# Performance work log

Hardware: AMD Instinct MI355X
Metric: run time of the kernel (lower is better)

Reference implementation:

```python
import jax, jax.numpy as jnp
import numpy as np

B, N, H = 8, 2048, 256

def setup_inputs() -> dict:
    key = jax.random.key(0)
    k1, k2, k3, k4, k5 = jax.random.split(key, 5)
    h = jax.random.normal(k1, (B, N, H), dtype=jnp.float32)
    node_mask = jnp.ones((B, N, 1), dtype=jnp.float32)
    n_nodes = N  # unused by the forward math, kept for signature fidelity
    s1 = 1.0 / np.sqrt(H)
    W1 = jax.random.uniform(k2, (H, H), minval=-s1, maxval=s1, dtype=jnp.float32)
    b1 = jax.random.uniform(k3, (H,), minval=-s1, maxval=s1, dtype=jnp.float32)
    w2 = jax.random.uniform(k4, (H,), minval=-s1, maxval=s1, dtype=jnp.float32)
    b2 = jax.random.uniform(k5, (), minval=-s1, maxval=s1, dtype=jnp.float32)
    return {"h": h, "node_mask": node_mask, "n_nodes": n_nodes,
            "W1": W1, "b1": b1, "w2": w2, "b2": b2}

def reference(h, node_mask, n_nodes, W1, b1, w2, b2):
    # node_dec: Linear + SiLU
    x = jax.nn.silu(jnp.einsum('bnh,oh->bno', h, W1) + b1)  # [B,N,H]
    # pre_di applied to pairwise difference is linear, so factor:
    # pre_di(x_i - x_j) = (x_i @ w2) - (x_j @ w2) + b2
    s = jnp.einsum('bnh,h->bn', x, w2)                       # [B,N]
    out = s[:, :, None] - s[:, None, :] + b2                 # [B,N,N]
    return out.astype(jnp.int64)                             # torch .long() truncates
```

## Files before the change

### kernel.cpp

```cpp
#include <hip/hip_runtime.h>
#include <math.h>

#define B_ 8
#define N_ 2048
#define H_ 256

typedef double d4 __attribute__((ext_vector_type(4)));

__global__ __launch_bounds__(256)
void transpose_w1(const float* __restrict__ W1, float* __restrict__ W1T) {
    W1T[(size_t)blockIdx.x * H_ + threadIdx.x] =
        W1[(size_t)threadIdx.x * H_ + blockIdx.x];
}

__device__ __forceinline__ int self_probe_var() {
    const int l = threadIdx.x & 63;
    d4 z = {0.0, 0.0, 0.0, 0.0};
    d4 r1 = __builtin_amdgcn_mfma_f64_16x16x4f64((double)(l + 1), 1.0, z, 0, 0, 0);
    d4 r2 = __builtin_amdgcn_mfma_f64_16x16x4f64(1.0, (double)(l + 1), z, 0, 0, 0);
    d4 r3 = __builtin_amdgcn_mfma_f64_16x16x4f64((double)(l & 15), 1.0, z, 0, 0, 0);
    const double pw0 = __shfl(r1[0], 0, 64);
    const double pw1 = __shfl(r2[0], 0, 64);
    const double pw2 = __shfl(r3[0], 1, 64);
    const double pw3 = __shfl(r3[2], 16, 64);
    const double pw4 = __shfl(r2[2], 16, 64);
    if (pw0 != 100.0 || pw1 != 100.0) return 0;
    if (pw2 == 0.0 && pw3 == 24.0)  return 1;
    if (pw2 == 0.0 && pw3 == 36.0)  return 3;
    if (pw2 == 4.0 && pw4 == 124.0) return 2;
    if (pw2 == 4.0 && pw4 == 136.0) return 4;
    return 0;
}

__global__ __launch_bounds__(256)
__attribute__((amdgpu_waves_per_eu(2, 4)))
void s_mfma_uni(const float* __restrict__ hp, const float* __restrict__ W1T,
                const float* __restrict__ b1, const float* __restrict__ w2,
                double* __restrict__ s_out) {
    const int var = self_probe_var();
    if (var == 0) return;
    __shared__ double spart[4][32];
    const int t = threadIdx.x;
    const int lane = t & 63;
    const int wave = __builtin_amdgcn_readfirstlane(t >> 6);
    const int a15 = lane & 15, g = lane >> 4;
    const int m0 = blockIdx.x * 32;
    const int oc = wave * 64;
    const float* ap0 = hp + (size_t)(m0 + a15) * H_ + g;
    const float* ap1 = hp + (size_t)(m0 + 16 + a15) * H_ + g;
    const float* bp  = W1T + (size_t)g * H_ + oc + a15;

    d4 acc[2][4];
    #pragma unroll
    for (int mt = 0; mt < 2; ++mt)
        #pragma unroll
        for (int ot = 0; ot < 4; ++ot) acc[mt][ot] = (d4){0.0, 0.0, 0.0, 0.0};

    float ac[4], an[4];
    float bcv[8], bnv[8];
    ac[0] = ap0[0]; ac[1] = ap0[4]; ac[2] = ap1[0]; ac[3] = ap1[4];
    #pragma unroll
    for (int ot = 0; ot < 4; ++ot) {
        bcv[ot]     = bp[ot * 16];
        bcv[4 + ot] = bp[4 * H_ + ot * 16];
    }

    for (int kc = 0; kc < H_; kc += 8) {
        const int kn = (kc + 8 < H_) ? (kc + 8) : 0;
        an[0] = ap0[kn]; an[1] = ap0[kn + 4];
        an[2] = ap1[kn]; an[3] = ap1[kn + 4];
        #pragma unroll
        for (int ot = 0; ot < 4; ++ot) {
            bnv[ot]     = bp[(size_t)kn * H_ + ot * 16];
            bnv[4 + ot] = bp[(size_t)(kn + 4) * H_ + ot * 16];
        }
        {
            const double a0 = (double)ac[0], a1 = (double)ac[2];
            #pragma unroll
            for (int ot = 0; ot < 4; ++ot) {
                const double bv = (double)bcv[ot];
                acc[0][ot] = __builtin_amdgcn_mfma_f64_16x16x4f64(a0, bv, acc[0][ot], 0, 0, 0);
                acc[1][ot] = __builtin_amdgcn_mfma_f64_16x16x4f64(a1, bv, acc[1][ot], 0, 0, 0);
            }
        }
        {
            const double a0 = (double)ac[1], a1 = (double)ac[3];
            #pragma unroll
            for (int ot = 0; ot < 4; ++ot) {
                const double bv = (double)bcv[4 + ot];
                acc[0][ot] = __builtin_amdgcn_mfma_f64_16x16x4f64(a0, bv, acc[0][ot], 0, 0, 0);
                acc[1][ot] = __builtin_amdgcn_mfma_f64_16x16x4f64(a1, bv, acc[1][ot], 0, 0, 0);
            }
        }
        #pragma unroll
        for (int q = 0; q < 4; ++q) ac[q] = an[q];
        #pragma unroll
        for (int q = 0; q < 8; ++q) bcv[q] = bnv[q];
    }

    if (var == 1 || var == 3) {
        double psum[2][4];
        #pragma unroll
        for (int mt = 0; mt < 2; ++mt)
            #pragma unroll
            for (int v = 0; v < 4; ++v) psum[mt][v] = 0.0;
        #pragma unroll
        for (int ot = 0; ot < 4; ++ot) {
            const int o = oc + ot * 16 + a15;
            const double bb = (double)b1[o];
            const double ww = (double)w2[o];
            #pragma unroll
            for (int mt = 0; mt < 2; ++mt)
                #pragma unroll
                for (int v = 0; v < 4; ++v) {
                    const double u = acc[mt][ot][v] + bb;
                    psum[mt][v] += ww * (u / (1.0 + exp(-u)));
                }
        }
        #pragma unroll
        for (int mt = 0; mt < 2; ++mt)
            #pragma unroll
            for (int v = 0; v < 4; ++v) {
                double x = psum[mt][v];
                x += __shfl_xor(x, 1, 64);
                x += __shfl_xor(x, 2, 64);
                x += __shfl_xor(x, 4, 64);
                x += __shfl_xor(x, 8, 64);
                psum[mt][v] = x;
            }
        if (a15 == 0) {
            #pragma unroll
            for (int mt = 0; mt < 2; ++mt)
                #pragma unroll
                for (int v = 0; v < 4; ++v) {
                    const int row = (var == 1) ? (4 * g + v) : (g + 4 * v);
                    spart[wave][mt * 16 + row] = psum[mt][v];
                }
        }
    } else {
        double ps[2] = {0.0, 0.0};
        #pragma unroll
        for (int ot = 0; ot < 4; ++ot)
            #pragma unroll
            for (int v = 0; v < 4; ++v) {
                const int cv = (var == 2) ? (4 * g + v) : (g + 4 * v);
                const int o = oc + ot * 16 + cv;
                const double bb = (double)b1[o];
                const double ww = (double)w2[o];
                #pragma unroll
                for (int mt = 0; mt < 2; ++mt) {
                    const double u = acc[mt][ot][v] + bb;
                    ps[mt] += ww * (u / (1.0 + exp(-u)));
                }
            }
        #pragma unroll
        for (int mt = 0; mt < 2; ++mt) {
            ps[mt] += __shfl_xor(ps[mt], 16, 64);
            ps[mt] += __shfl_xor(ps[mt], 32, 64);
        }
        if (g == 0) {
            spart[wave][a15]      = ps[0];
            spart[wave][16 + a15] = ps[1];
        }
    }
    __syncthreads();
    if (t < 32)
        s_out[m0 + t] = spart[0][t] + spart[1][t] + spart[2][t] + spart[3][t];
}

__global__ __launch_bounds__(256)
__attribute__((amdgpu_waves_per_eu(2, 4)))
void s_valu_kernel(const float* __restrict__ hp, const float* __restrict__ W1T,
                   const float* __restrict__ b1, const float* __restrict__ w2,
                   double* __restrict__ s_out) {
    if (self_probe_var() != 0) return;
    const int t = threadIdx.x;
    const int lane = t & 63;
    const int wave = __builtin_amdgcn_readfirstlane(t >> 6);
    const int m0 = blockIdx.x * 16 + wave * 4;
    const int o0 = lane * 4;
    const float* hr = hp + (size_t)m0 * H_;
    const float* wp = W1T + o0;

    double acc[4][4];
    #pragma unroll
    for (int j = 0; j < 4; ++j)
        #pragma unroll
        for (int r = 0; r < 4; ++r) acc[j][r] = 0.0;

    float4 wA[8], wB[8];
    float hA[32], hB[32];

    #define LOADW(dst, kcv)                                                   \
        do {                                                                  \
            _Pragma("unroll")                                                 \
            for (int kk = 0; kk < 8; ++kk)                                    \
                dst[kk] = *reinterpret_cast<const float4*>(                   \
                    wp + (size_t)((kcv) + kk) * H_);                          \
        } while (0)

    #define LOADH(dst, kcv)                                                   \
        do {                                                                  \
            _Pragma("unroll")                                                 \
            for (int r = 0; r < 4; ++r)                                       \
                _Pragma("unroll")                                             \
                for (int kk = 0; kk < 8; ++kk)                                \
                    dst[r * 8 + kk] = hr[r * H_ + (kcv) + kk];                \
        } while (0)

    #define COMPUTE(wv, hbuf)                                                 \
        do {                                                                  \
            _Pragma("unroll")                                                 \
            for (int kk = 0; kk < 8; ++kk) {                                  \
                const double h0 = (double)hbuf[0 * 8 + kk];                   \
                const double h1 = (double)hbuf[1 * 8 + kk];                   \
                const double h2 = (double)hbuf[2 * 8 + kk];                   \
                const double h3 = (double)hbuf[3 * 8 + kk];                   \
                const double a0 = (double)wv[kk].x;                           \
                const double a1 = (double)wv[kk].y;                           \
                const double a2 = (double)wv[kk].z;                           \
                const double a3 = (double)wv[kk].w;                           \
                acc[0][0] = fma(a0, h0, acc[0][0]);                           \
                acc[0][1] = fma(a0, h1, acc[0][1]);                           \
                acc[0][2] = fma(a0, h2, acc[0][2]);                           \
                acc[0][3] = fma(a0, h3, acc[0][3]);                           \
                acc[1][0] = fma(a1, h0, acc[1][0]);                           \
                acc[1][1] = fma(a1, h1, acc[1][1]);                           \
                acc[1][2] = fma(a1, h2, acc[1][2]);                           \
                acc[1][3] = fma(a1, h3, acc[1][3]);                           \
                acc[2][0] = fma(a2, h0, acc[2][0]);                           \
                acc[2][1] = fma(a2, h1, acc[2][1]);                           \
                acc[2][2] = fma(a2, h2, acc[2][2]);                           \
                acc[2][3] = fma(a2, h3, acc[2][3]);                           \
                acc[3][0] = fma(a3, h0, acc[3][0]);                           \
                acc[3][1] = fma(a3, h1, acc[3][1]);                           \
                acc[3][2] = fma(a3, h2, acc[3][2]);                           \
                acc[3][3] = fma(a3, h3, acc[3][3]);                           \
            }                                                                 \
        } while (0)

    LOADW(wA, 0);
    LOADH(hA, 0);
    for (int kc = 0; kc < H_; kc += 16) {
        LOADW(wB, kc + 8);
        LOADH(hB, kc + 8);
        COMPUTE(wA, hA);
        if (kc + 16 < H_) {
            LOADW(wA, kc + 16);
            LOADH(hA, kc + 16);
        }
        COMPUTE(wB, hB);
    }
    #undef LOADW
    #undef LOADH
    #undef COMPUTE

    const float4 b1v = *reinterpret_cast<const float4*>(b1 + o0);
    const float4 w2v = *reinterpret_cast<const float4*>(w2 + o0);
    double psum[4] = {0.0, 0.0, 0.0, 0.0};
    #define EPI(j, bc, wc)                                                    \
        do {                                                                  \
            const double bb = (double)bc, ww = (double)wc;                    \
            _Pragma("unroll")                                                 \
            for (int r = 0; r < 4; ++r) {                                     \
                const double u = acc[j][r] + bb;                              \
                psum[r] += ww * (u / (1.0 + exp(-u)));                        \
            }                                                                 \
        } while (0)
    EPI(0, b1v.x, w2v.x);
    EPI(1, b1v.y, w2v.y);
    EPI(2, b1v.z, w2v.z);
    EPI(3, b1v.w, w2v.w);
    #undef EPI

    #pragma unroll
    for (int r = 0; r < 4; ++r) {
        double v = psum[r];
        v += __shfl_xor(v, 1, 64);
        v += __shfl_xor(v, 2, 64);
        v += __shfl_xor(v, 4, 64);
        v += __shfl_xor(v, 8, 64);
        v += __shfl_xor(v, 16, 64);
        v += __shfl_xor(v, 32, 64);
        if (lane == 0) s_out[m0 + r] = v;
    }
}

__global__ __launch_bounds__(256)
void pair_kernel(const double* __restrict__ s, const float* __restrict__ b2p,
                 int* __restrict__ out) {
    const double b2 = (double)b2p[0];
    const unsigned total4 = (unsigned)(B_) * (unsigned)(N_) * (unsigned)(N_) / 4u;
    const unsigned stride = gridDim.x * blockDim.x;
    for (unsigned idx = blockIdx.x * blockDim.x + threadIdx.x; idx < total4;
         idx += stride) {
        const unsigned base = idx * 4u;
        const unsigned bi  = base >> 22;
        const unsigned rem = base & ((1u << 22) - 1u);
        const unsigned i   = rem >> 11;
        const unsigned j   = rem & (N_ - 1u);
        const double si = s[bi * N_ + i];
        const double* sp = s + bi * N_ + j;
        const double sj0 = sp[0], sj1 = sp[1], sj2 = sp[2], sj3 = sp[3];
        int4 o;
        o.x = (int)trunc((si - sj0) + b2);
        o.y = (int)trunc((si - sj1) + b2);
        o.z = (int)trunc((si - sj2) + b2);
        o.w = (int)trunc((si - sj3) + b2);
        *reinterpret_cast<int4*>(out + base) = o;
    }
}

extern "C" void kernel_launch(void* const* d_in, const int* in_sizes, int n_in,
                              void* d_out, int out_size, void* d_ws, size_t ws_size,
                              hipStream_t stream) {
    const float* hp = (const float*)d_in[0];
    const float* W1 = (const float*)d_in[3];
    const float* b1 = (const float*)d_in[4];
    const float* w2 = (const float*)d_in[5];
    const float* b2 = (const float*)d_in[6];

    float*  W1T = (float*)d_ws;
    double* s   = (double*)((char*)d_ws + H_ * H_ * sizeof(float));
    int* out = (int*)d_out;

    transpose_w1<<<H_, H_, 0, stream>>>(W1, W1T);
    s_mfma_uni<<<(B_ * N_) / 32, 256, 0, stream>>>(hp, W1T, b1, w2, s);
    s_valu_kernel<<<(B_ * N_) / 16, 256, 0, stream>>>(hp, W1T, b1, w2, s);
    pair_kernel<<<2048, 256, 0, stream>>>(s, b2, out);
}
```

Baseline: 74.62 us.

## Pack W1 into a per-lane contiguous layout for float4 B-operand loads

Adds a pack_w1 kernel that reorders W1 rows so that each lane's K-slices for its output column sit contiguously. The MFMA GEMM loop can then fetch B operands with float4 loads over 16 chunks instead of strided scalar loads, and the K indexing is permuted so each lane covers k = g + 4*(...) groups. The intent is fewer, wider memory instructions in the inner loop. The cost is an extra launch and more workspace, and the per-lane A loads become strided by 4 floats.

```diff
diff --git a/kernel.cpp b/kernel.cpp
--- a/kernel.cpp
+++ b/kernel.cpp
@@ -11,6 +11,12 @@
 void transpose_w1(const float* __restrict__ W1, float* __restrict__ W1T) {
     W1T[(size_t)blockIdx.x * H_ + threadIdx.x] =
         W1[(size_t)threadIdx.x * H_ + blockIdx.x];
+}
+
+__global__ __launch_bounds__(256)
+void pack_w1(const float* __restrict__ W1, float* __restrict__ W1P) {
+    const int o = blockIdx.x, k = threadIdx.x;
+    W1P[(size_t)o * H_ + (k & 3) * 64 + (k >> 2)] = W1[(size_t)o * H_ + k];
 }
 
 __device__ __forceinline__ int self_probe_var() {
@@ -34,7 +40,7 @@
 
 __global__ __launch_bounds__(256)
 __attribute__((amdgpu_waves_per_eu(2, 4)))
-void s_mfma_uni(const float* __restrict__ hp, const float* __restrict__ W1T,
+void s_mfma_uni(const float* __restrict__ hp, const float* __restrict__ W1P,
                 const float* __restrict__ b1, const float* __restrict__ w2,
                 double* __restrict__ s_out) {
     const int var = self_probe_var();
@@ -47,8 +53,8 @@
     const int m0 = blockIdx.x * 32;
     const int oc = wave * 64;
     const float* ap0 = hp + (size_t)(m0 + a15) * H_ + g;
-    const float* ap1 = hp + (size_t)(m0 + 16 + a15) * H_ + g;
-    const float* bp  = W1T + (size_t)g * H_ + oc + a15;
+    const float* ap1 = ap0 + 16 * H_;
+    const float* bq = W1P + ((size_t)(oc + a15) * 4 + g) * 64;
 
     d4 acc[2][4];
     #pragma unroll
@@ -56,47 +62,64 @@
         #pragma unroll
         for (int ot = 0; ot < 4; ++ot) acc[mt][ot] = (d4){0.0, 0.0, 0.0, 0.0};
 
-    float ac[4], an[4];
-    float bcv[8], bnv[8];
-    ac[0] = ap0[0]; ac[1] = ap0[4]; ac[2] = ap1[0]; ac[3] = ap1[4];
-    #pragma unroll
-    for (int ot = 0; ot < 4; ++ot) {
-        bcv[ot]     = bp[ot * 16];
-        bcv[4 + ot] = bp[4 * H_ + ot * 16];
-    }
-
-    for (int kc = 0; kc < H_; kc += 8) {
-        const int kn = (kc + 8 < H_) ? (kc + 8) : 0;
-        an[0] = ap0[kn]; an[1] = ap0[kn + 4];
-        an[2] = ap1[kn]; an[3] = ap1[kn + 4];
-        #pragma unroll
-        for (int ot = 0; ot < 4; ++ot) {
-            bnv[ot]     = bp[(size_t)kn * H_ + ot * 16];
-            bnv[4 + ot] = bp[(size_t)(kn + 4) * H_ + ot * 16];
-        }
-        {
-            const double a0 = (double)ac[0], a1 = (double)ac[2];
-            #pragma unroll
-            for (int ot = 0; ot < 4; ++ot) {
-                const double bv = (double)bcv[ot];
-                acc[0][ot] = __builtin_amdgcn_mfma_f64_16x16x4f64(a0, bv, acc[0][ot], 0, 0, 0);
-                acc[1][ot] = __builtin_amdgcn_mfma_f64_16x16x4f64(a1, bv, acc[1][ot], 0, 0, 0);
-            }
-        }
-        {
-            const double a0 = (double)ac[1], a1 = (double)ac[3];
-            #pragma unroll
-            for (int ot = 0; ot < 4; ++ot) {
-                const double bv = (double)bcv[4 + ot];
-                acc[0][ot] = __builtin_amdgcn_mfma_f64_16x16x4f64(a0, bv, acc[0][ot], 0, 0, 0);
-                acc[1][ot] = __builtin_amdgcn_mfma_f64_16x16x4f64(a1, bv, acc[1][ot], 0, 0, 0);
-            }
-        }
-        #pragma unroll
-        for (int q = 0; q < 4; ++q) ac[q] = an[q];
-        #pragma unroll
-        for (int q = 0; q < 8; ++q) bcv[q] = bnv[q];
-    }
+    float4 bc[4], bn[4];
+    float ac[8], an[8];
+
+    #define LOADB(dst, c)                                                     \
+        do {                                                                  \
+            _Pragma("unroll")                                                 \
+            for (int ot = 0; ot < 4; ++ot)                                    \
+                dst[ot] = *reinterpret_cast<const float4*>(                   \
+                    bq + ot * 16 * H_ * 4 / 4 * 4 / 4 + 0);                   \
+        } while (0)
+    #undef LOADB
+    #define LOADB(dst, c)                                                     \
+        do {                                                                  \
+            _Pragma("unroll")                                                 \
+            for (int ot = 0; ot < 4; ++ot)                                    \
+                dst[ot] = *reinterpret_cast<const float4*>(                   \
+                    bq + (size_t)ot * 4096 + (c) * 4);                        \
+        } while (0)
+
+    #define LOADA(dst, c)                                                     \
+        do {                                                                  \
+            _Pragma("unroll")                                                 \
+            for (int q = 0; q < 4; ++q) {                                     \
+                dst[q]     = ap0[(c) * 16 + q * 4];                           \
+                dst[4 + q] = ap1[(c) * 16 + q * 4];                           \
+            }                                                                 \
+        } while (0)
+
+    LOADB(bc, 0);
+    LOADA(ac, 0);
+    for (int c = 0; c < 16; ++c) {
+        const int cn = (c + 1 < 16) ? (c + 1) : 0;
+        LOADB(bn, cn);
+        LOADA(an, cn);
+        #pragma unroll
+        for (int q = 0; q < 4; ++q) {
+            const double a0 = (double)ac[q];
+            const double a1 = (double)ac[4 + q];
+            const double b0 = (double)((const float*)&bc[0])[q];
+            const double b1v = (double)((const float*)&bc[1])[q];
+            const double b2v = (double)((const float*)&bc[2])[q];
+            const double b3v = (double)((const float*)&bc[3])[q];
+            acc[0][0] = __builtin_amdgcn_mfma_f64_16x16x4f64(a0, b0,  acc[0][0], 0, 0, 0);
+            acc[1][0] = __builtin_amdgcn_mfma_f64_16x16x4f64(a1, b0,  acc[1][0], 0, 0, 0);
+            acc[0][1] = __builtin_amdgcn_mfma_f64_16x16x4f64(a0, b1v, acc[0][1], 0, 0, 0);
+            acc[1][1] = __builtin_amdgcn_mfma_f64_16x16x4f64(a1, b1v, acc[1][1], 0, 0, 0);
+            acc[0][2] = __builtin_amdgcn_mfma_f64_16x16x4f64(a0, b2v, acc[0][2], 0, 0, 0);
+            acc[1][2] = __builtin_amdgcn_mfma_f64_16x16x4f64(a1, b2v, acc[1][2], 0, 0, 0);
+            acc[0][3] = __builtin_amdgcn_mfma_f64_16x16x4f64(a0, b3v, acc[0][3], 0, 0, 0);
+            acc[1][3] = __builtin_amdgcn_mfma_f64_16x16x4f64(a1, b3v, acc[1][3], 0, 0, 0);
+        }
+        #pragma unroll
+        for (int q = 0; q < 8; ++q) ac[q] = an[q];
+        #pragma unroll
+        for (int q = 0; q < 4; ++q) bc[q] = bn[q];
+    }
+    #undef LOADB
+    #undef LOADA
 
     if (var == 1 || var == 3) {
         double psum[2][4];
@@ -321,11 +344,13 @@
     const float* b2 = (const float*)d_in[6];
 
     float*  W1T = (float*)d_ws;
-    double* s   = (double*)((char*)d_ws + H_ * H_ * sizeof(float));
+    float*  W1P = (float*)((char*)d_ws + 256 * 1024);
+    double* s   = (double*)((char*)d_ws + 512 * 1024);
     int* out = (int*)d_out;
 
     transpose_w1<<<H_, H_, 0, stream>>>(W1, W1T);
-    s_mfma_uni<<<(B_ * N_) / 32, 256, 0, stream>>>(hp, W1T, b1, w2, s);
+    pack_w1<<<H_, H_, 0, stream>>>(W1, W1P);
+    s_mfma_uni<<<(B_ * N_) / 32, 256, 0, stream>>>(hp, W1P, b1, w2, s);
     s_valu_kernel<<<(B_ * N_) / 16, 256, 0, stream>>>(hp, W1T, b1, w2, s);
     pair_kernel<<<2048, 256, 0, stream>>>(s, b2, out);
 }
```

Measured after the change: 89.49 us. 19.9% more time.

## Split K across two wave groups in fp64 MFMA kernel with LDS reduction

Applied to the files above, without the earlier changes.

Doubles the block to 512 threads and splits the 256-wide K dimension between two groups of four waves. Each group accumulates half of the fp64 MFMA products, and the first group writes its partials to a 64KB LDS buffer that the second group adds before the SiLU and w2 epilogue. The goal is to halve the serial MFMA chain per wave and raise latency hiding. In exchange it adds an LDS round trip, an extra barrier and a large shared-memory footprint that may cap occupancy.

```diff
diff --git a/kernel.cpp b/kernel.cpp
--- a/kernel.cpp
+++ b/kernel.cpp
@@ -32,23 +32,27 @@
     return 0;
 }
 
-__global__ __launch_bounds__(256)
+__global__ __launch_bounds__(512)
 __attribute__((amdgpu_waves_per_eu(2, 4)))
 void s_mfma_uni(const float* __restrict__ hp, const float* __restrict__ W1T,
                 const float* __restrict__ b1, const float* __restrict__ w2,
                 double* __restrict__ s_out) {
     const int var = self_probe_var();
     if (var == 0) return;
+    __shared__ double u_lds[4][32][64];
     __shared__ double spart[4][32];
     const int t = threadIdx.x;
     const int lane = t & 63;
-    const int wave = __builtin_amdgcn_readfirstlane(t >> 6);
+    const int w = __builtin_amdgcn_readfirstlane(t >> 6);
+    const int kh = w >> 2;
+    const int ow = w & 3;
     const int a15 = lane & 15, g = lane >> 4;
     const int m0 = blockIdx.x * 32;
-    const int oc = wave * 64;
-    const float* ap0 = hp + (size_t)(m0 + a15) * H_ + g;
-    const float* ap1 = hp + (size_t)(m0 + 16 + a15) * H_ + g;
-    const float* bp  = W1T + (size_t)g * H_ + oc + a15;
+    const int oc = ow * 64;
+    const int K0 = kh * 128;
+    const float* ap0 = hp + (size_t)(m0 + a15) * H_ + g + K0;
+    const float* ap1 = ap0 + 16 * H_;
+    const float* bp  = W1T + (size_t)(K0 + g) * H_ + oc + a15;
 
     d4 acc[2][4];
     #pragma unroll
@@ -65,8 +69,8 @@
         bcv[4 + ot] = bp[4 * H_ + ot * 16];
     }
 
-    for (int kc = 0; kc < H_; kc += 8) {
-        const int kn = (kc + 8 < H_) ? (kc + 8) : 0;
+    for (int kc = 0; kc < 128; kc += 8) {
+        const int kn = (kc + 8 < 128) ? (kc + 8) : 0;
         an[0] = ap0[kn]; an[1] = ap0[kn + 4];
         an[2] = ap1[kn]; an[3] = ap1[kn + 4];
         #pragma unroll
@@ -98,69 +102,89 @@
         for (int q = 0; q < 8; ++q) bcv[q] = bnv[q];
     }
 
-    if (var == 1 || var == 3) {
-        double psum[2][4];
+    if (kh == 0) {
         #pragma unroll
         for (int mt = 0; mt < 2; ++mt)
             #pragma unroll
-            for (int v = 0; v < 4; ++v) psum[mt][v] = 0.0;
-        #pragma unroll
-        for (int ot = 0; ot < 4; ++ot) {
-            const int o = oc + ot * 16 + a15;
-            const double bb = (double)b1[o];
-            const double ww = (double)w2[o];
+            for (int ot = 0; ot < 4; ++ot)
+                #pragma unroll
+                for (int v = 0; v < 4; ++v)
+                    u_lds[ow][mt * 16 + ot * 4 + v][lane] = acc[mt][ot][v];
+    }
+    __syncthreads();
+    if (kh == 1) {
+        #pragma unroll
+        for (int mt = 0; mt < 2; ++mt)
+            #pragma unroll
+            for (int ot = 0; ot < 4; ++ot)
+                #pragma unroll
+                for (int v = 0; v < 4; ++v)
+                    acc[mt][ot][v] += u_lds[ow][mt * 16 + ot * 4 + v][lane];
+
+        if (var == 1 || var == 3) {
+            double psum[2][4];
             #pragma unroll
             for (int mt = 0; mt < 2; ++mt)
                 #pragma unroll
-                for (int v = 0; v < 4; ++v) {
-                    const double u = acc[mt][ot][v] + bb;
-                    psum[mt][v] += ww * (u / (1.0 + exp(-u)));
-                }
-        }
-        #pragma unroll
-        for (int mt = 0; mt < 2; ++mt)
-            #pragma unroll
-            for (int v = 0; v < 4; ++v) {
-                double x = psum[mt][v];
-                x += __shfl_xor(x, 1, 64);
-                x += __shfl_xor(x, 2, 64);
-                x += __shfl_xor(x, 4, 64);
-                x += __shfl_xor(x, 8, 64);
-                psum[mt][v] = x;
-            }
-        if (a15 == 0) {
-            #pragma unroll
-            for (int mt = 0; mt < 2; ++mt)
-                #pragma unroll
-                for (int v = 0; v < 4; ++v) {
-                    const int row = (var == 1) ? (4 * g + v) : (g + 4 * v);
-                    spart[wave][mt * 16 + row] = psum[mt][v];
-                }
-        }
-    } else {
-        double ps[2] = {0.0, 0.0};
-        #pragma unroll
-        for (int ot = 0; ot < 4; ++ot)
-            #pragma unroll
-            for (int v = 0; v < 4; ++v) {
-                const int cv = (var == 2) ? (4 * g + v) : (g + 4 * v);
-                const int o = oc + ot * 16 + cv;
+                for (int v = 0; v < 4; ++v) psum[mt][v] = 0.0;
+            #pragma unroll
+            for (int ot = 0; ot < 4; ++ot) {
+                const int o = oc + ot * 16 + a15;
                 const double bb = (double)b1[o];
                 const double ww = (double)w2[o];
                 #pragma unroll
-                for (int mt = 0; mt < 2; ++mt) {
-                    const double u = acc[mt][ot][v] + bb;
-                    ps[mt] += ww * (u / (1.0 + exp(-u)));
+                for (int mt = 0; mt < 2; ++mt)
+                    #pragma unroll
+                    for (int v = 0; v < 4; ++v) {
+                        const double u = acc[mt][ot][v] + bb;
+                        psum[mt][v] += ww * (u / (1.0 + exp(-u)));
+                    }
+            }
+            #pragma unroll
+            for (int mt = 0; mt < 2; ++mt)
+                #pragma unroll
+                for (int v = 0; v < 4; ++v) {
+                    double x = psum[mt][v];
+                    x += __shfl_xor(x, 1, 64);
+                    x += __shfl_xor(x, 2, 64);
+                    x += __shfl_xor(x, 4, 64);
+                    x += __shfl_xor(x, 8, 64);
+                    psum[mt][v] = x;
                 }
-            }
-        #pragma unroll
-        for (int mt = 0; mt < 2; ++mt) {
-            ps[mt] += __shfl_xor(ps[mt], 16, 64);
-            ps[mt] += __shfl_xor(ps[mt], 32, 64);
-        }
-        if (g == 0) {
-            spart[wave][a15]      = ps[0];
-            spart[wave][16 + a15] = ps[1];
+            if (a15 == 0) {
+                #pragma unroll
+                for (int mt = 0; mt < 2; ++mt)
+                    #pragma unroll
+                    for (int v = 0; v < 4; ++v) {
+                        const int row = (var == 1) ? (4 * g + v) : (g + 4 * v);
+                        spart[ow][mt * 16 + row] = psum[mt][v];
+                    }
+            }
+        } else {
+            double ps[2] = {0.0, 0.0};
+            #pragma unroll
+            for (int ot = 0; ot < 4; ++ot)
+                #pragma unroll
+                for (int v = 0; v < 4; ++v) {
+                    const int cv = (var == 2) ? (4 * g + v) : (g + 4 * v);
+                    const int o = oc + ot * 16 + cv;
+                    const double bb = (double)b1[o];
+                    const double ww = (double)w2[o];
+                    #pragma unroll
+                    for (int mt = 0; mt < 2; ++mt) {
+                        const double u = acc[mt][ot][v] + bb;
+                        ps[mt] += ww * (u / (1.0 + exp(-u)));
+                    }
+                }
+            #pragma unroll
+            for (int mt = 0; mt < 2; ++mt) {
+                ps[mt] += __shfl_xor(ps[mt], 16, 64);
+                ps[mt] += __shfl_xor(ps[mt], 32, 64);
+            }
+            if (g == 0) {
+                spart[ow][a15]      = ps[0];
+                spart[ow][16 + a15] = ps[1];
+            }
         }
     }
     __syncthreads();
@@ -321,11 +345,11 @@
     const float* b2 = (const float*)d_in[6];
 
     float*  W1T = (float*)d_ws;
-    double* s   = (double*)((char*)d_ws + H_ * H_ * sizeof(float));
+    double* s   = (double*)((char*)d_ws + 256 * 1024);
     int* out = (int*)d_out;
 
     transpose_w1<<<H_, H_, 0, stream>>>(W1, W1T);
-    s_mfma_uni<<<(B_ * N_) / 32, 256, 0, stream>>>(hp, W1T, b1, w2, s);
+    s_mfma_uni<<<(B_ * N_) / 32, 512, 0, stream>>>(hp, W1T, b1, w2, s);
     s_valu_kernel<<<(B_ * N_) / 16, 256, 0, stream>>>(hp, W1T, b1, w2, s);
     pair_kernel<<<2048, 256, 0, stream>>>(s, b2, out);
 }
```

Result: slower. 80.14 us (+7.4%).

## Merge MFMA and VALU s-kernels into one launch with runtime path selection

Applied to the files above, without the earlier changes.

Two kernels, an MFMA path and a VALU fallback, each ran a hardware probe and exited early if the probe chose the other path. They are now one kernel that probes once and branches, which removes one launch. The VALU fallback is retiled to 8 rows per wave with 4-k steps so it fits the 32-row block of the merged grid. The s buffer offset in workspace is also changed to a fixed 256 KiB.

```diff
diff --git a/kernel.cpp b/kernel.cpp
--- a/kernel.cpp
+++ b/kernel.cpp
@@ -34,255 +34,238 @@
 
 __global__ __launch_bounds__(256)
 __attribute__((amdgpu_waves_per_eu(2, 4)))
-void s_mfma_uni(const float* __restrict__ hp, const float* __restrict__ W1T,
-                const float* __restrict__ b1, const float* __restrict__ w2,
-                double* __restrict__ s_out) {
+void s_kernel(const float* __restrict__ hp, const float* __restrict__ W1T,
+              const float* __restrict__ b1, const float* __restrict__ w2,
+              double* __restrict__ s_out) {
+    __shared__ double spart[4][32];
     const int var = self_probe_var();
-    if (var == 0) return;
-    __shared__ double spart[4][32];
     const int t = threadIdx.x;
     const int lane = t & 63;
     const int wave = __builtin_amdgcn_readfirstlane(t >> 6);
-    const int a15 = lane & 15, g = lane >> 4;
     const int m0 = blockIdx.x * 32;
-    const int oc = wave * 64;
-    const float* ap0 = hp + (size_t)(m0 + a15) * H_ + g;
-    const float* ap1 = hp + (size_t)(m0 + 16 + a15) * H_ + g;
-    const float* bp  = W1T + (size_t)g * H_ + oc + a15;
-
-    d4 acc[2][4];
-    #pragma unroll
-    for (int mt = 0; mt < 2; ++mt)
+
+    if (var != 0) {
+        const int a15 = lane & 15, g = lane >> 4;
+        const int oc = wave * 64;
+        const float* ap0 = hp + (size_t)(m0 + a15) * H_ + g;
+        const float* ap1 = ap0 + 16 * H_;
+        const float* bp  = W1T + (size_t)g * H_ + oc + a15;
+
+        d4 acc[2][4];
         #pragma unroll
-        for (int ot = 0; ot < 4; ++ot) acc[mt][ot] = (d4){0.0, 0.0, 0.0, 0.0};
-
-    float ac[4], an[4];
-    float bcv[8], bnv[8];
-    ac[0] = ap0[0]; ac[1] = ap0[4]; ac[2] = ap1[0]; ac[3] = ap1[4];
-    #pragma unroll
-    for (int ot = 0; ot < 4; ++ot) {
-        bcv[ot]     = bp[ot * 16];
-        bcv[4 + ot] = bp[4 * H_ + ot * 16];
-    }
-
-    for (int kc = 0; kc < H_; kc += 8) {
-        const int kn = (kc + 8 < H_) ? (kc + 8) : 0;
-        an[0] = ap0[kn]; an[1] = ap0[kn + 4];
-        an[2] = ap1[kn]; an[3] = ap1[kn + 4];
+        for (int mt = 0; mt < 2; ++mt)
+            #pragma unroll
+            for (int ot = 0; ot < 4; ++ot) acc[mt][ot] = (d4){0.0, 0.0, 0.0, 0.0};
+
+        float ac[4], an[4];
+        float bcv[8], bnv[8];
+        ac[0] = ap0[0]; ac[1] = ap0[4]; ac[2] = ap1[0]; ac[3] = ap1[4];
         #pragma unroll
         for (int ot = 0; ot < 4; ++ot) {
-            bnv[ot]     = bp[(size_t)kn * H_ + ot * 16];
-            bnv[4 + ot] = bp[(size_t)(kn + 4) * H_ + ot * 16];
-        }
-        {
-            const double a0 = (double)ac[0], a1 = (double)ac[2];
+            bcv[ot]     = bp[ot * 16];
+            bcv[4 + ot] = bp[4 * H_ + ot * 16];
+        }
+
+        for (int kc = 0; kc < H_; kc += 8) {
+            const int kn = (kc + 8 < H_) ? (kc + 8) : 0;
+            an[0] = ap0[kn]; an[1] = ap0[kn + 4];
+            an[2] = ap1[kn]; an[3] = ap1[kn + 4];
             #pragma unroll
             for (int ot = 0; ot < 4; ++ot) {
-                const double bv = (double)bcv[ot];
-                acc[0][ot] = __builtin_amdgcn_mfma_f64_16x16x4f64(a0, bv, acc[0][ot], 0, 0, 0);
-                acc[1][ot] = __builtin_amdgcn_mfma_f64_16x16x4f64(a1, bv, acc[1][ot], 0, 0, 0);
-            }
-        }
-        {
-            const double a0 = (double)ac[1], a1 = (double)ac[3];
+                bnv[ot]     = bp[(size_t)kn * H_ + ot * 16];
+                bnv[4 + ot] = bp[(size_t)(kn + 4) * H_ + ot * 16];
+            }
+            {
+                const double a0 = (double)ac[0], a1 = (double)ac[2];
+                #pragma unroll
+                for (int ot = 0; ot < 4; ++ot) {
+                    const double bv = (double)bcv[ot];
+                    acc[0][ot] = __builtin_amdgcn_mfma_f64_16x16x4f64(a0, bv, acc[0][ot], 0, 0, 0);
+                    acc[1][ot] = __builtin_amdgcn_mfma_f64_16x16x4f64(a1, bv, acc[1][ot], 0, 0, 0);
+                }
+            }
+            {
+                const double a0 = (double)ac[1], a1 = (double)ac[3];
+                #pragma unroll
+                for (int ot = 0; ot < 4; ++ot) {
+                    const double bv = (double)bcv[4 + ot];
+                    acc[0][ot] = __builtin_amdgcn_mfma_f64_16x16x4f64(a0, bv, acc[0][ot], 0, 0, 0);
+                    acc[1][ot] = __builtin_amdgcn_mfma_f64_16x16x4f64(a1, bv, acc[1][ot], 0, 0, 0);
+                }
+            }
+            #pragma unroll
+            for (int q = 0; q < 4; ++q) ac[q] = an[q];
+            #pragma unroll
+            for (int q = 0; q < 8; ++q) bcv[q] = bnv[q];
+        }
+
+        if (var == 1 || var == 3) {
+            double psum[2][4];
+            #pragma unroll
+            for (int mt = 0; mt < 2; ++mt)
+                #pragma unroll
+                for (int v = 0; v < 4; ++v) psum[mt][v] = 0.0;
             #pragma unroll
             for (int ot = 0; ot < 4; ++ot) {
-                const double bv = (double)bcv[4 + ot];
-                acc[0][ot] = __builtin_amdgcn_mfma_f64_16x16x4f64(a0, bv, acc[0][ot], 0, 0, 0);
-                acc[1][ot] = __builtin_amdgcn_mfma_f64_16x16x4f64(a1, bv, acc[1][ot], 0, 0, 0);
-            }
-        }
-        #pragma unroll
-        for (int q = 0; q < 4; ++q) ac[q] = an[q];
-        #pragma unroll
-        for (int q = 0; q < 8; ++q) bcv[q] = bnv[q];
-    }
-
-    if (var == 1 || var == 3) {
-        double psum[2][4];
-        #pragma unroll
-        for (int mt = 0; mt < 2; ++mt)
-            #pragma unroll
-            for (int v = 0; v < 4; ++v) psum[mt][v] = 0.0;
-        #pragma unroll
-        for (int ot = 0; ot < 4; ++ot) {
-            const int o = oc + ot * 16 + a15;
-            const double bb = (double)b1[o];
-            const double ww = (double)w2[o];
-            #pragma unroll
-            for (int mt = 0; mt < 2; ++mt)
-                #pragma unroll
-                for (int v = 0; v < 4; ++v) {
-                    const double u = acc[mt][ot][v] + bb;
-                    psum[mt][v] += ww * (u / (1.0 + exp(-u)));
-                }
-        }
-        #pragma unroll
-        for (int mt = 0; mt < 2; ++mt)
-            #pragma unroll
-            for (int v = 0; v < 4; ++v) {
-                double x = psum[mt][v];
-                x += __shfl_xor(x, 1, 64);
-                x += __shfl_xor(x, 2, 64);
-                x += __shfl_xor(x, 4, 64);
-                x += __shfl_xor(x, 8, 64);
-                psum[mt][v] = x;
-            }
-        if (a15 == 0) {
-            #pragma unroll
-            for (int mt = 0; mt < 2; ++mt)
-                #pragma unroll
-                for (int v = 0; v < 4; ++v) {
-                    const int row = (var == 1) ? (4 * g + v) : (g + 4 * v);
-                    spart[wave][mt * 16 + row] = psum[mt][v];
-                }
-        }
-    } else {
-        double ps[2] = {0.0, 0.0};
-        #pragma unroll
-        for (int ot = 0; ot < 4; ++ot)
-            #pragma unroll
-            for (int v = 0; v < 4; ++v) {
-                const int cv = (var == 2) ? (4 * g + v) : (g + 4 * v);
-                const int o = oc + ot * 16 + cv;
+                const int o = oc + ot * 16 + a15;
                 const double bb = (double)b1[o];
                 const double ww = (double)w2[o];
                 #pragma unroll
-                for (int mt = 0; mt < 2; ++mt) {
-                    const double u = acc[mt][ot][v] + bb;
-                    ps[mt] += ww * (u / (1.0 + exp(-u)));
+                for (int mt = 0; mt < 2; ++mt)
+                    #pragma unroll
+                    for (int v = 0; v < 4; ++v) {
+                        const double u = acc[mt][ot][v] + bb;
+                        psum[mt][v] += ww * (u / (1.0 + exp(-u)));
+                    }
+            }
+            #pragma unroll
+            for (int mt = 0; mt < 2; ++mt)
+                #pragma unroll
+                for (int v = 0; v < 4; ++v) {
+                    double x = psum[mt][v];
+                    x += __shfl_xor(x, 1, 64);
+                    x += __shfl_xor(x, 2, 64);
+                    x += __shfl_xor(x, 4, 64);
+                    x += __shfl_xor(x, 8, 64);
+                    psum[mt][v] = x;
                 }
-            }
+            if (a15 == 0) {
+                #pragma unroll
+                for (int mt = 0; mt < 2; ++mt)
+                    #pragma unroll
+                    for (int v = 0; v < 4; ++v) {
+                        const int row = (var == 1) ? (4 * g + v) : (g + 4 * v);
+                        spart[wave][mt * 16 + row] = psum[mt][v];
+                    }
+            }
+        } else {
+            double ps[2] = {0.0, 0.0};
+            #pragma unroll
+            for (int ot = 0; ot < 4; ++ot)
+                #pragma unroll
+                for (int v = 0; v < 4; ++v) {
+                    const int cv = (var == 2) ? (4 * g + v) : (g + 4 * v);
+                    const int o = oc + ot * 16 + cv;
+                    const double bb = (double)b1[o];
+                    const double ww = (double)w2[o];
+                    #pragma unroll
+                    for (int mt = 0; mt < 2; ++mt) {
+                        const double u = acc[mt][ot][v] + bb;
+                        ps[mt] += ww * (u / (1.0 + exp(-u)));
+                    }
+                }
+            #pragma unroll
+            for (int mt = 0; mt < 2; ++mt) {
+                ps[mt] += __shfl_xor(ps[mt], 16, 64);
+                ps[mt] += __shfl_xor(ps[mt], 32, 64);
+            }
+            if (g == 0) {
+                spart[wave][a15]      = ps[0];
+                spart[wave][16 + a15] = ps[1];
+            }
+        }
+        __syncthreads();
+        if (t < 32)
+            s_out[m0 + t] = spart[0][t] + spart[1][t] + spart[2][t] + spart[3][t];
+        return;
+    }
+
+    {
+        const int mv0 = m0 + wave * 8;
+        const int o0 = lane * 4;
+        const float* hr = hp + (size_t)mv0 * H_;
+        const float* wp = W1T + o0;
+
+        double acc[4][8];
         #pragma unroll
-        for (int mt = 0; mt < 2; ++mt) {
-            ps[mt] += __shfl_xor(ps[mt], 16, 64);
-            ps[mt] += __shfl_xor(ps[mt], 32, 64);
-        }
-        if (g == 0) {
-            spart[wave][a15]      = ps[0];
-            spart[wave][16 + a15] = ps[1];
-        }
-    }
-    __syncthreads();
-    if (t < 32)
-        s_out[m0 + t] = spart[0][t] + spart[1][t] + spart[2][t] + spart[3][t];
-}
-
-__global__ __launch_bounds__(256)
-__attribute__((amdgpu_waves_per_eu(2, 4)))
-void s_valu_kernel(const float* __restrict__ hp, const float* __restrict__ W1T,
-                   const float* __restrict__ b1, const float* __restrict__ w2,
-                   double* __restrict__ s_out) {
-    if (self_probe_var() != 0) return;
-    const int t = threadIdx.x;
-    const int lane = t & 63;
-    const int wave = __builtin_amdgcn_readfirstlane(t >> 6);
-    const int m0 = blockIdx.x * 16 + wave * 4;
-    const int o0 = lane * 4;
-    const float* hr = hp + (size_t)m0 * H_;
-    const float* wp = W1T + o0;
-
-    double acc[4][4];
-    #pragma unroll
-    for (int j = 0; j < 4; ++j)
+        for (int j = 0; j < 4; ++j)
+            #pragma unroll
+            for (int r = 0; r < 8; ++r) acc[j][r] = 0.0;
+
+        float4 wA[4], wB[4];
+        float hA[32], hB[32];
+
+        #define VLOADW(dst, kcv)                                              \
+            do {                                                              \
+                _Pragma("unroll")                                             \
+                for (int kk = 0; kk < 4; ++kk)                                \
+                    dst[kk] = *reinterpret_cast<const float4*>(               \
+                        wp + (size_t)((kcv) + kk) * H_);                      \
+            } while (0)
+
+        #define VLOADH(dst, kcv)                                              \
+            do {                                                              \
+                _Pragma("unroll")                                             \
+                for (int r = 0; r < 8; ++r)                                   \
+                    _Pragma("unroll")                                         \
+                    for (int kk = 0; kk < 4; ++kk)                            \
+                        dst[r * 4 + kk] = hr[r * H_ + (kcv) + kk];            \
+            } while (0)
+
+        #define VCOMPUTE(wv, hbuf)                                            \
+            do {                                                              \
+                _Pragma("unroll")                                             \
+                for (int kk = 0; kk < 4; ++kk) {                              \
+                    const double a0 = (double)wv[kk].x;                       \
+                    const double a1 = (double)wv[kk].y;                       \
+                    const double a2 = (double)wv[kk].z;                       \
+                    const double a3 = (double)wv[kk].w;                       \
+                    _Pragma("unroll")                                         \
+                    for (int r = 0; r < 8; ++r) {                             \
+                        const double hv = (double)hbuf[r * 4 + kk];           \
+                        acc[0][r] = fma(a0, hv, acc[0][r]);                   \
+                        acc[1][r] = fma(a1, hv, acc[1][r]);                   \
+                        acc[2][r] = fma(a2, hv, acc[2][r]);                   \
+                        acc[3][r] = fma(a3, hv, acc[3][r]);                   \
+                    }                                                         \
+                }                                                             \
+            } while (0)
+
+        VLOADW(wA, 0);
+        VLOADH(hA, 0);
+        for (int kc = 0; kc < H_; kc += 8) {
+            VLOADW(wB, kc + 4);
+            VLOADH(hB, kc + 4);
+            VCOMPUTE(wA, hA);
+            if (kc + 8 < H_) {
+                VLOADW(wA, kc + 8);
+                VLOADH(hA, kc + 8);
+            }
+            VCOMPUTE(wB, hB);
+        }
+        #undef VLOADW
+        #undef VLOADH
+        #undef VCOMPUTE
+
+        const float4 b1v = *reinterpret_cast<const float4*>(b1 + o0);
+        const float4 w2v = *reinterpret_cast<const float4*>(w2 + o0);
+        double psum[8] = {0.0, 0.0, 0.0, 0.0, 0.0, 0.0, 0.0, 0.0};
+        #define VEPI(j, bc, wc)                                               \
+            do {                                                              \
+                const double bb = (double)bc, ww = (double)wc;                \
+                _Pragma("unroll")                                             \
+                for (int r = 0; r < 8; ++r) {                                 \
+                    const double u = acc[j][r] + bb;                          \
+                    psum[r] += ww * (u / (1.0 + exp(-u)));                    \
+                }                                                             \
+            } while (0)
+        VEPI(0, b1v.x, w2v.x);
+        VEPI(1, b1v.y, w2v.y);
+        VEPI(2, b1v.z, w2v.z);
+        VEPI(3, b1v.w, w2v.w);
+        #undef VEPI
+
         #pragma unroll
-        for (int r = 0; r < 4; ++r) acc[j][r] = 0.0;
-
-    float4 wA[8], wB[8];
-    float hA[32], hB[32];
-
-    #define LOADW(dst, kcv)                                                   \
-        do {                                                                  \
-            _Pragma("unroll")                                                 \
-            for (int kk = 0; kk < 8; ++kk)                                    \
-                dst[kk] = *reinterpret_cast<const float4*>(                   \
-                    wp + (size_t)((kcv) + kk) * H_);                          \
-        } while (0)
-
-    #define LOADH(dst, kcv)                                                   \
-        do {                                                                  \
-            _Pragma("unroll")                                                 \
-            for (int r = 0; r < 4; ++r)                                       \
-                _Pragma("unroll")                                             \
-                for (int kk = 0; kk < 8; ++kk)                                \
-                    dst[r * 8 + kk] = hr[r * H_ + (kcv) + kk];                \
-        } while (0)
-
-    #define COMPUTE(wv, hbuf)                                                 \
-        do {                                                                  \
-            _Pragma("unroll")                                                 \
-            for (int kk = 0; kk < 8; ++kk) {                                  \
-                const double h0 = (double)hbuf[0 * 8 + kk];                   \
-                const double h1 = (double)hbuf[1 * 8 + kk];                   \
-                const double h2 = (double)hbuf[2 * 8 + kk];                   \
-                const double h3 = (double)hbuf[3 * 8 + kk];                   \
-                const double a0 = (double)wv[kk].x;                           \
-                const double a1 = (double)wv[kk].y;                           \
-                const double a2 = (double)wv[kk].z;                           \
-                const double a3 = (double)wv[kk].w;                           \
-                acc[0][0] = fma(a0, h0, acc[0][0]);                           \
-                acc[0][1] = fma(a0, h1, acc[0][1]);                           \
-                acc[0][2] = fma(a0, h2, acc[0][2]);                           \
-                acc[0][3] = fma(a0, h3, acc[0][3]);                           \
-                acc[1][0] = fma(a1, h0, acc[1][0]);                           \
-                acc[1][1] = fma(a1, h1, acc[1][1]);                           \
-                acc[1][2] = fma(a1, h2, acc[1][2]);                           \
-                acc[1][3] = fma(a1, h3, acc[1][3]);                           \
-                acc[2][0] = fma(a2, h0, acc[2][0]);                           \
-                acc[2][1] = fma(a2, h1, acc[2][1]);                           \
-                acc[2][2] = fma(a2, h2, acc[2][2]);                           \
-                acc[2][3] = fma(a2, h3, acc[2][3]);                           \
-                acc[3][0] = fma(a3, h0, acc[3][0]);                           \
-                acc[3][1] = fma(a3, h1, acc[3][1]);                           \
-                acc[3][2] = fma(a3, h2, acc[3][2]);                           \
-                acc[3][3] = fma(a3, h3, acc[3][3]);                           \
-            }                                                                 \
-        } while (0)
-
-    LOADW(wA, 0);
-    LOADH(hA, 0);
-    for (int kc = 0; kc < H_; kc += 16) {
-        LOADW(wB, kc + 8);
-        LOADH(hB, kc + 8);
-        COMPUTE(wA, hA);
-        if (kc + 16 < H_) {
-            LOADW(wA, kc + 16);
-            LOADH(hA, kc + 16);
-        }
-        COMPUTE(wB, hB);
-    }
-    #undef LOADW
-    #undef LOADH
-    #undef COMPUTE
-
-    const float4 b1v = *reinterpret_cast<const float4*>(b1 + o0);
-    const float4 w2v = *reinterpret_cast<const float4*>(w2 + o0);
-    double psum[4] = {0.0, 0.0, 0.0, 0.0};
-    #define EPI(j, bc, wc)                                                    \
-        do {                                                                  \
-            const double bb = (double)bc, ww = (double)wc;                    \
-            _Pragma("unroll")                                                 \
-            for (int r = 0; r < 4; ++r) {                                     \
-                const double u = acc[j][r] + bb;                              \
-                psum[r] += ww * (u / (1.0 + exp(-u)));                        \
-            }                                                                 \
-        } while (0)
-    EPI(0, b1v.x, w2v.x);
-    EPI(1, b1v.y, w2v.y);
-    EPI(2, b1v.z, w2v.z);
-    EPI(3, b1v.w, w2v.w);
-    #undef EPI
-
-    #pragma unroll
-    for (int r = 0; r < 4; ++r) {
-        double v = psum[r];
-        v += __shfl_xor(v, 1, 64);
-        v += __shfl_xor(v, 2, 64);
-        v += __shfl_xor(v, 4, 64);
-        v += __shfl_xor(v, 8, 64);
-        v += __shfl_xor(v, 16, 64);
-        v += __shfl_xor(v, 32, 64);
-        if (lane == 0) s_out[m0 + r] = v;
+        for (int r = 0; r < 8; ++r) {
+            double v = psum[r];
+            v += __shfl_xor(v, 1, 64);
+            v += __shfl_xor(v, 2, 64);
+            v += __shfl_xor(v, 4, 64);
+            v += __shfl_xor(v, 8, 64);
+            v += __shfl_xor(v, 16, 64);
+            v += __shfl_xor(v, 32, 64);
+            if (lane == 0) s_out[mv0 + r] = v;
+        }
     }
 }
 
@@ -321,11 +304,10 @@
     const float* b2 = (const float*)d_in[6];
 
     float*  W1T = (float*)d_ws;
-    double* s   = (double*)((char*)d_ws + H_ * H_ * sizeof(float));
+    double* s   = (double*)((char*)d_ws + 256 * 1024);
     int* out = (int*)d_out;
 
     transpose_w1<<<H_, H_, 0, stream>>>(W1, W1T);
-    s_mfma_uni<<<(B_ * N_) / 32, 256, 0, stream>>>(hp, W1T, b1, w2, s);
-    s_valu_kernel<<<(B_ * N_) / 16, 256, 0, stream>>>(hp, W1T, b1, w2, s);
+    s_kernel<<<(B_ * N_) / 32, 256, 0, stream>>>(hp, W1T, b1, w2, s);
     pair_kernel<<<2048, 256, 0, stream>>>(s, b2, out);
 }
```

Result: faster. 72.57 us (median of 2 runs) (-2.8%).
